# Kernel optimization log

Hardware: AMD Instinct MI355X
Metric: run time of the kernel (lower is better)

Reference implementation:

```python
import jax, jax.numpy as jnp
import numpy as np

BETA = 0.25


def setup_inputs() -> dict:
    key = jax.random.key(0)
    k1, k2 = jax.random.split(key)
    latents = jax.random.normal(k1, (16, 4096, 256), dtype=jnp.float32)
    K = 1024
    # torch init: uniform(-1/K, 1/K)
    codebook = jax.random.uniform(k2, (K, 256), dtype=jnp.float32, minval=-1.0 / K, maxval=1.0 / K)
    return {"latents": latents, "codebook": codebook}


def reference(latents, codebook):
    D = codebook.shape[1]
    flat = latents.reshape(-1, D)  # [N, D]
    dist = (jnp.sum(flat * flat, axis=1, keepdims=True)
            + jnp.sum(codebook * codebook, axis=1)
            - 2.0 * jnp.matmul(flat, codebook.T))
    encoding_inds = jnp.argmin(dist, axis=1)  # [N]
    # gather nearest codebook vectors (equivalent to one-hot @ codebook)
    quantized = codebook[encoding_inds].reshape(latents.shape)
    commitment_loss = jnp.mean((jax.lax.stop_gradient(quantized) - latents) ** 2)
    embedding_loss = jnp.mean((quantized - jax.lax.stop_gradient(latents)) ** 2)
    vq_loss = commitment_loss * BETA + embedding_loss
    # straight-through estimator
    quantized_st = latents + jax.lax.stop_gradient(quantized - latents)
    return quantized_st, vq_loss
```

## Files before the change

kernel.cpp:

```cpp
#include <hip/hip_runtime.h>

typedef __attribute__((ext_vector_type(4))) float f32x4;
typedef __attribute__((ext_vector_type(2))) long i64x2;

#define SCALE 262144.0f
#define NEG2S -524288.0f
#define INV_S2 1.4551915228366852e-11f
#define OFFS35 34359738368.0f

static __device__ __forceinline__ unsigned umin2(unsigned a, unsigned b) { return a < b ? a : b; }

static __device__ __forceinline__ float dec_e4m3(unsigned b) {
  int e = (b >> 3) & 15, m = b & 7;
  float v = e ? ldexpf((float)(8 + m), e - 10) : ldexpf((float)m, -9);
  return (b & 0x80) ? -v : v;
}

__global__ void vq_prep(const float* __restrict__ cb,
                        float* __restrict__ norms,
                        unsigned char* __restrict__ cbh,
                        float* __restrict__ loss_out) {
  if (blockIdx.x == 0 && threadIdx.x == 0) *loss_out = 0.0f;
  const int lane = threadIdx.x & 63;
  const int code = (blockIdx.x * blockDim.x + threadIdx.x) >> 6;
  const f32x4 v = ((const f32x4*)(cb + (long)code * 256))[lane];
  unsigned w = __builtin_amdgcn_cvt_pk_fp8_f32(v[0] * SCALE, v[1] * SCALE, 0, false);
  w = __builtin_amdgcn_cvt_pk_fp8_f32(v[2] * SCALE, v[3] * SCALE, w, true);
  float n = 0.f;
#pragma unroll
  for (int j = 0; j < 4; ++j) {
    float d = dec_e4m3((w >> (8 * j)) & 0xFFu);
    n = __builtin_fmaf(d, d, n);
  }
  const int newpos = ((lane >> 1) & 3) * 64 + (lane >> 3) * 8 + (lane & 1) * 4;
  *(unsigned*)(cbh + (long)code * 256 + newpos) = w;
#pragma unroll
  for (int m = 1; m < 64; m <<= 1) n += __shfl_xor(n, m);
  if (lane == 0) norms[code] = n + OFFS35;
}

#define BM 128
#define DD 256
#define NTHR 512
#define NSUB 16

__global__ __launch_bounds__(NTHR, 4)
void vq_main(const float* __restrict__ X,
             const float* __restrict__ CB,
             const float* __restrict__ norms_g,
             const unsigned char* __restrict__ cbh,
             float* __restrict__ out,
             float* __restrict__ loss_out,
             float lscale) {
  __shared__ __attribute__((aligned(16))) unsigned char Eb[2 * 16384];
  __shared__ __attribute__((aligned(16))) float nrmLds[1024];
  __shared__ unsigned keys[BM];
  __shared__ float wsumX[8];
  __shared__ float wsumS[8];

  const int t = threadIdx.x;
  const int lane = t & 63;
  const int wave = t >> 6;
  const int wr = wave >> 1;
  const int wc = wave & 1;
  const int lo16 = lane & 15;
  const int hi = lane >> 4;
  const long rowBase = (long)blockIdx.x * BM;

  const char* cbB = (const char*)cbh;
  char* ebBase = (char*)Eb;
#define STAGE_E(ST, BUF)                                                                      \
  {                                                                                           \
    _Pragma("unroll") for (int c = 0; c < 2; ++c) {                                           \
      unsigned o = (unsigned)(wave * 2048 + c * 1024 + lane * 16);                            \
      unsigned src = o ^ ((((o >> 8) & 7u)) << 4);                                            \
      __builtin_amdgcn_global_load_lds(                                                       \
          (const __attribute__((address_space(1))) void*)(cbB + (unsigned)(ST)*16384u + src), \
          (__attribute__((address_space(3))) void*)(ebBase + (unsigned)(BUF)*16384u + wave * 2048 + c * 1024), \
          16, 0, 0);                                                                          \
    }                                                                                         \
  }

  STAGE_E(0, 0);

  nrmLds[t] = norms_g[t];
  nrmLds[t + 512] = norms_g[t + 512];
  if (t < BM) keys[t] = 0xFFFFFFFFu;

  float xn = 0.f;
  long a[2][8];
#pragma unroll
  for (int s = 0; s < 2; ++s) {
    const f32x4* xr = (const f32x4*)(X + (rowBase + wr * 32 + s * 16 + lo16) * DD);
#pragma unroll
    for (int ks = 0; ks < 8; ++ks) {
      f32x4 v0 = __builtin_nontemporal_load(xr + ks * 8 + hi * 2);
      f32x4 v1 = __builtin_nontemporal_load(xr + ks * 8 + hi * 2 + 1);
#pragma unroll
      for (int j = 0; j < 4; ++j) xn = __builtin_fmaf(v0[j], v0[j], xn);
#pragma unroll
      for (int j = 0; j < 4; ++j) xn = __builtin_fmaf(v1[j], v1[j], xn);
      unsigned w0 = __builtin_amdgcn_cvt_pk_fp8_f32(v0[0], v0[1], 0, false);
      w0 = __builtin_amdgcn_cvt_pk_fp8_f32(v0[2], v0[3], w0, true);
      unsigned w1 = __builtin_amdgcn_cvt_pk_fp8_f32(v1[0], v1[1], 0, false);
      w1 = __builtin_amdgcn_cvt_pk_fp8_f32(v1[2], v1[3], w1, true);
      a[s][ks] = (long)w0 | ((long)w1 << 32);
    }
  }
  __syncthreads();

  unsigned best[2][4];
#pragma unroll
  for (int s = 0; s < 2; ++s)
#pragma unroll
    for (int r = 0; r < 4; ++r) best[s][r] = 0xFFFFFFFFu;

  const unsigned swzl = (unsigned)((lo16 & 7) << 4);
  unsigned nbase[2];
#pragma unroll
  for (int n = 0; n < 2; ++n) nbase[n] = (unsigned)((wc * 32 + n * 16 + lo16) * 256) ^ swzl;
  const unsigned hi64 = (unsigned)(hi * 64);

  for (int st = 0; st < NSUB; ++st) {
    if (st + 1 < NSUB) {
      STAGE_E(st + 1, (st + 1) & 1);
      asm volatile("s_waitcnt vmcnt(2)" ::: "memory");
    } else {
      asm volatile("s_waitcnt vmcnt(0)" ::: "memory");
    }
    __builtin_amdgcn_s_barrier();
    __builtin_amdgcn_sched_barrier(0);

    const char* eb = ebBase + (st & 1) * 16384;
    f32x4 acc[2][2];
#pragma unroll
    for (int s = 0; s < 2; ++s)
#pragma unroll
      for (int n = 0; n < 2; ++n) {
        f32x4 z = {0.f, 0.f, 0.f, 0.f};
        acc[s][n] = z;
      }

#pragma unroll
    for (int kp = 0; kp < 4; ++kp) {
      const unsigned koff = hi64 + (unsigned)(kp * 16);
      i64x2 b0 = *(const i64x2*)(eb + (nbase[0] ^ koff));
      i64x2 b1 = *(const i64x2*)(eb + (nbase[1] ^ koff));
      __builtin_amdgcn_sched_barrier(0);
      __builtin_amdgcn_s_barrier();
      asm volatile("s_waitcnt lgkmcnt(0)" ::: "memory");
      __builtin_amdgcn_sched_barrier(0);
      __builtin_amdgcn_s_setprio(1);
      acc[0][0] = __builtin_amdgcn_mfma_f32_16x16x32_fp8_fp8(a[0][2 * kp], b0.x, acc[0][0], 0, 0, 0);
      acc[1][0] = __builtin_amdgcn_mfma_f32_16x16x32_fp8_fp8(a[1][2 * kp], b0.x, acc[1][0], 0, 0, 0);
      acc[0][1] = __builtin_amdgcn_mfma_f32_16x16x32_fp8_fp8(a[0][2 * kp], b1.x, acc[0][1], 0, 0, 0);
      acc[1][1] = __builtin_amdgcn_mfma_f32_16x16x32_fp8_fp8(a[1][2 * kp], b1.x, acc[1][1], 0, 0, 0);
      acc[0][0] = __builtin_amdgcn_mfma_f32_16x16x32_fp8_fp8(a[0][2 * kp + 1], b0.y, acc[0][0], 0, 0, 0);
      acc[1][0] = __builtin_amdgcn_mfma_f32_16x16x32_fp8_fp8(a[1][2 * kp + 1], b0.y, acc[1][0], 0, 0, 0);
      acc[0][1] = __builtin_amdgcn_mfma_f32_16x16x32_fp8_fp8(a[0][2 * kp + 1], b1.y, acc[0][1], 0, 0, 0);
      acc[1][1] = __builtin_amdgcn_mfma_f32_16x16x32_fp8_fp8(a[1][2 * kp + 1], b1.y, acc[1][1], 0, 0, 0);
      __builtin_amdgcn_s_setprio(0);
      __builtin_amdgcn_sched_barrier(0);
    }

#pragma unroll
    for (int n = 0; n < 2; ++n) {
      float nf = nrmLds[st * 64 + wc * 32 + n * 16 + lo16];
      unsigned code = (unsigned)(st * 64 + wc * 32 + n * 16 + lo16);
#pragma unroll
      for (int s = 0; s < 2; ++s)
#pragma unroll
        for (int r = 0; r < 4; ++r) {
          float sv = __builtin_fmaf(NEG2S, acc[s][n][r], nf);
          best[s][r] = umin2(best[s][r], (__float_as_uint(sv) & 0xFFFFFC00u) | code);
        }
    }
  }

#pragma unroll
  for (int s = 0; s < 2; ++s)
#pragma unroll
    for (int r = 0; r < 4; ++r) {
#pragma unroll
      for (int msk = 1; msk < 16; msk <<= 1)
        best[s][r] = umin2(best[s][r], (unsigned)__shfl_xor((int)best[s][r], msk));
    }
  if (lo16 == 0) {
#pragma unroll
    for (int s = 0; s < 2; ++s)
#pragma unroll
      for (int r = 0; r < 4; ++r) {
        atomicMin(&keys[wr * 32 + s * 16 + hi * 4 + r], best[s][r]);
      }
  }

#pragma unroll
  for (int msk = 1; msk < 64; msk <<= 1) xn += __shfl_xor(xn, msk);
  if (lane == 0) wsumX[wave] = wc ? 0.0f : xn;

  __syncthreads();

  float sc = 0.f;
  if (t < BM) {
    unsigned e = keys[t];
    float sr = __uint_as_float((e & 0xFFFFFC00u) | 512u) - OFFS35;
    sc = sr * INV_S2;
  }
#pragma unroll
  for (int msk = 1; msk < 64; msk <<= 1) sc += __shfl_xor(sc, msk);
  if (lane == 0) wsumS[wave] = sc;

  {
    const f32x4* CBv = (const f32x4*)CB;
    f32x4* Og = (f32x4*)(out + rowBase * DD);
#pragma unroll 4
    for (int i = 0; i < 16; ++i) {
      int idx = t + NTHR * i;
      int row = idx >> 6, d4 = idx & 63;
      int code = (int)(keys[row] & 1023u);
      f32x4 e = CBv[code * 64 + d4];
      __builtin_nontemporal_store(e, Og + idx);
    }
  }

  __syncthreads();
  if (t == 0) {
    float tot = 0.f;
#pragma unroll
    for (int w = 0; w < 8; ++w) tot += wsumX[w] + wsumS[w];
    atomicAdd(loss_out, tot * lscale);
  }
}

extern "C" void kernel_launch(void* const* d_in, const int* in_sizes, int n_in,
                              void* d_out, int out_size, void* d_ws, size_t ws_size,
                              hipStream_t stream) {
  const float* X = (const float*)d_in[0];
  const float* CB = (const float*)d_in[1];
  float* out = (float*)d_out;

  const int ND = in_sizes[0];
  const int K = in_sizes[1] / DD;
  const int N = ND / DD;

  float* ws_norms = (float*)d_ws;
  unsigned char* ws_cb = (unsigned char*)((char*)d_ws + 4096);
  float* loss_out = out + (size_t)ND;

  vq_prep<<<K / 4, 256, 0, stream>>>(CB, ws_norms, ws_cb, loss_out);

  const float lscale = 1.25f / (float)ND;
  vq_main<<<N / BM, NTHR, 0, stream>>>(X, CB, ws_norms, ws_cb, out, loss_out, lscale);
}
```

Measured before the change: 61.38 us.

## Load X once per block via LDS and halve per-substage barriers

Each wave now loads and converts a distinct 16-row slice of X to FP8 and stages it in a swizzled 32KB LDS buffer. The A fragments are then read back from LDS, which removes the duplicate global loads that the two column-waves previously issued for the same rows. The norm partial is now counted from every wave. The inner k-loop also groups four B reads per phase, so it runs two barrier and lgkmcnt waits per substage instead of four. The cost is 32KB more LDS per block, which may lower occupancy below the launch_bounds target of 4.

```diff
diff --git a/kernel.cpp b/kernel.cpp
--- a/kernel.cpp
+++ b/kernel.cpp
@@ -53,6 +53,7 @@
              float* __restrict__ loss_out,
              float lscale) {
   __shared__ __attribute__((aligned(16))) unsigned char Eb[2 * 16384];
+  __shared__ __attribute__((aligned(16))) unsigned char Xs[32768];
   __shared__ __attribute__((aligned(16))) float nrmLds[1024];
   __shared__ unsigned keys[BM];
   __shared__ float wsumX[8];
@@ -88,10 +89,11 @@
   if (t < BM) keys[t] = 0xFFFFFFFFu;
 
   float xn = 0.f;
-  long a[2][8];
-#pragma unroll
-  for (int s = 0; s < 2; ++s) {
-    const f32x4* xr = (const f32x4*)(X + (rowBase + wr * 32 + s * 16 + lo16) * DD);
+  {
+    const f32x4* xr = (const f32x4*)(X + (rowBase + wave * 16 + lo16) * DD);
+    const unsigned row = (unsigned)(wave * 16 + lo16);
+    const unsigned wbase = row * 256 + (unsigned)(hi * 64);
+    const unsigned swz3 = (row & 7u) << 3;
 #pragma unroll
     for (int ks = 0; ks < 8; ++ks) {
       f32x4 v0 = __builtin_nontemporal_load(xr + ks * 8 + hi * 2);
@@ -104,10 +106,21 @@
       w0 = __builtin_amdgcn_cvt_pk_fp8_f32(v0[2], v0[3], w0, true);
       unsigned w1 = __builtin_amdgcn_cvt_pk_fp8_f32(v1[0], v1[1], 0, false);
       w1 = __builtin_amdgcn_cvt_pk_fp8_f32(v1[2], v1[3], w1, true);
-      a[s][ks] = (long)w0 | ((long)w1 << 32);
+      *(long*)((char*)Xs + ((wbase + ks * 8) ^ swz3)) = (long)w0 | ((long)w1 << 32);
     }
   }
   __syncthreads();
+
+  long a[2][8];
+#pragma unroll
+  for (int s = 0; s < 2; ++s) {
+    const unsigned row = (unsigned)(wr * 32 + s * 16 + lo16);
+    const unsigned rbase = row * 256 + (unsigned)(hi * 64);
+    const unsigned swz3 = (row & 7u) << 3;
+#pragma unroll
+    for (int ks = 0; ks < 8; ++ks)
+      a[s][ks] = *(const long*)((const char*)Xs + ((rbase + ks * 8) ^ swz3));
+  }
 
   unsigned best[2][4];
 #pragma unroll
@@ -142,23 +155,34 @@
       }
 
 #pragma unroll
-    for (int kp = 0; kp < 4; ++kp) {
-      const unsigned koff = hi64 + (unsigned)(kp * 16);
-      i64x2 b0 = *(const i64x2*)(eb + (nbase[0] ^ koff));
-      i64x2 b1 = *(const i64x2*)(eb + (nbase[1] ^ koff));
+    for (int ph = 0; ph < 2; ++ph) {
+      const unsigned k0 = hi64 + (unsigned)(ph * 32);
+      i64x2 b0a = *(const i64x2*)(eb + (nbase[0] ^ k0));
+      i64x2 b1a = *(const i64x2*)(eb + (nbase[1] ^ k0));
+      i64x2 b0b = *(const i64x2*)(eb + (nbase[0] ^ (k0 + 16)));
+      i64x2 b1b = *(const i64x2*)(eb + (nbase[1] ^ (k0 + 16)));
       __builtin_amdgcn_sched_barrier(0);
       __builtin_amdgcn_s_barrier();
       asm volatile("s_waitcnt lgkmcnt(0)" ::: "memory");
       __builtin_amdgcn_sched_barrier(0);
       __builtin_amdgcn_s_setprio(1);
-      acc[0][0] = __builtin_amdgcn_mfma_f32_16x16x32_fp8_fp8(a[0][2 * kp], b0.x, acc[0][0], 0, 0, 0);
-      acc[1][0] = __builtin_amdgcn_mfma_f32_16x16x32_fp8_fp8(a[1][2 * kp], b0.x, acc[1][0], 0, 0, 0);
-      acc[0][1] = __builtin_amdgcn_mfma_f32_16x16x32_fp8_fp8(a[0][2 * kp], b1.x, acc[0][1], 0, 0, 0);
-      acc[1][1] = __builtin_amdgcn_mfma_f32_16x16x32_fp8_fp8(a[1][2 * kp], b1.x, acc[1][1], 0, 0, 0);
-      acc[0][0] = __builtin_amdgcn_mfma_f32_16x16x32_fp8_fp8(a[0][2 * kp + 1], b0.y, acc[0][0], 0, 0, 0);
-      acc[1][0] = __builtin_amdgcn_mfma_f32_16x16x32_fp8_fp8(a[1][2 * kp + 1], b0.y, acc[1][0], 0, 0, 0);
-      acc[0][1] = __builtin_amdgcn_mfma_f32_16x16x32_fp8_fp8(a[0][2 * kp + 1], b1.y, acc[0][1], 0, 0, 0);
-      acc[1][1] = __builtin_amdgcn_mfma_f32_16x16x32_fp8_fp8(a[1][2 * kp + 1], b1.y, acc[1][1], 0, 0, 0);
+      const int kb = 4 * ph;
+      acc[0][0] = __builtin_amdgcn_mfma_f32_16x16x32_fp8_fp8(a[0][kb], b0a.x, acc[0][0], 0, 0, 0);
+      acc[1][0] = __builtin_amdgcn_mfma_f32_16x16x32_fp8_fp8(a[1][kb], b0a.x, acc[1][0], 0, 0, 0);
+      acc[0][1] = __builtin_amdgcn_mfma_f32_16x16x32_fp8_fp8(a[0][kb], b1a.x, acc[0][1], 0, 0, 0);
+      acc[1][1] = __builtin_amdgcn_mfma_f32_16x16x32_fp8_fp8(a[1][kb], b1a.x, acc[1][1], 0, 0, 0);
+      acc[0][0] = __builtin_amdgcn_mfma_f32_16x16x32_fp8_fp8(a[0][kb + 1], b0a.y, acc[0][0], 0, 0, 0);
+      acc[1][0] = __builtin_amdgcn_mfma_f32_16x16x32_fp8_fp8(a[1][kb + 1], b0a.y, acc[1][0], 0, 0, 0);
+      acc[0][1] = __builtin_amdgcn_mfma_f32_16x16x32_fp8_fp8(a[0][kb + 1], b1a.y, acc[0][1], 0, 0, 0);
+      acc[1][1] = __builtin_amdgcn_mfma_f32_16x16x32_fp8_fp8(a[1][kb + 1], b1a.y, acc[1][1], 0, 0, 0);
+      acc[0][0] = __builtin_amdgcn_mfma_f32_16x16x32_fp8_fp8(a[0][kb + 2], b0b.x, acc[0][0], 0, 0, 0);
+      acc[1][0] = __builtin_amdgcn_mfma_f32_16x16x32_fp8_fp8(a[1][kb + 2], b0b.x, acc[1][0], 0, 0, 0);
+      acc[0][1] = __builtin_amdgcn_mfma_f32_16x16x32_fp8_fp8(a[0][kb + 2], b1b.x, acc[0][1], 0, 0, 0);
+      acc[1][1] = __builtin_amdgcn_mfma_f32_16x16x32_fp8_fp8(a[1][kb + 2], b1b.x, acc[1][1], 0, 0, 0);
+      acc[0][0] = __builtin_amdgcn_mfma_f32_16x16x32_fp8_fp8(a[0][kb + 3], b0b.y, acc[0][0], 0, 0, 0);
+      acc[1][0] = __builtin_amdgcn_mfma_f32_16x16x32_fp8_fp8(a[1][kb + 3], b0b.y, acc[1][0], 0, 0, 0);
+      acc[0][1] = __builtin_amdgcn_mfma_f32_16x16x32_fp8_fp8(a[0][kb + 3], b1b.y, acc[0][1], 0, 0, 0);
+      acc[1][1] = __builtin_amdgcn_mfma_f32_16x16x32_fp8_fp8(a[1][kb + 3], b1b.y, acc[1][1], 0, 0, 0);
       __builtin_amdgcn_s_setprio(0);
       __builtin_amdgcn_sched_barrier(0);
     }
@@ -196,7 +220,7 @@
 
 #pragma unroll
   for (int msk = 1; msk < 64; msk <<= 1) xn += __shfl_xor(xn, msk);
-  if (lane == 0) wsumX[wave] = wc ? 0.0f : xn;
+  if (lane == 0) wsumX[wave] = xn;
 
   __syncthreads();
 
```

New measurement: 53.50 us. 1.15x faster.
